# Optimization experiments

Hardware: AMD Instinct MI355X
Metric: run time of the kernel (lower is better)

## Reference

```python
import jax, jax.numpy as jnp
import numpy as np

EMB = 512
HEADS = 8

def setup_inputs() -> dict:
    key = jax.random.key(0)
    ks = jax.random.split(key, 6)
    x = jax.random.normal(ks[0], (8, 1024, EMB), dtype=jnp.float32)
    s = EMB ** -0.5
    Wq = jax.random.normal(ks[1], (EMB, EMB), dtype=jnp.float32) * s
    Wk = jax.random.normal(ks[2], (EMB, EMB), dtype=jnp.float32) * s
    Wv = jax.random.normal(ks[3], (EMB, EMB), dtype=jnp.float32) * s
    ln_gamma = jnp.ones((EMB,), dtype=jnp.float32)
    ln_beta = jnp.zeros((EMB,), dtype=jnp.float32)
    return {"x": x, "Wq": Wq, "Wk": Wk, "Wv": Wv, "ln_gamma": ln_gamma, "ln_beta": ln_beta}

def reference(x, Wq, Wk, Wv, ln_gamma, ln_beta):
    B, S, E = x.shape
    H = HEADS
    D = E // H
    scale = E ** -0.5  # note: source scales by emb_size**-0.5, not head_dim
    # projections (bias=False, torch Linear: x @ W.T)
    q = (x @ Wq.T).reshape(B, S, H, D).transpose(0, 2, 1, 3)  # [B,H,S,D]
    k = (x @ Wk.T).reshape(B, S, H, D).transpose(0, 2, 1, 3)
    v = (x @ Wv.T).reshape(B, S, H, D).transpose(0, 2, 1, 3)
    attn = jnp.einsum('bhqd,bhkd->bhqk', q, k) * scale
    attn = jax.nn.softmax(attn, axis=-1)
    out = jnp.einsum('bhqk,bhkd->bhqd', attn, v)
    out = out.transpose(0, 2, 1, 3).reshape(B, S, E)
    # LayerNorm (eps=1e-5, torch default)
    mu = jnp.mean(out, axis=-1, keepdims=True)
    var = jnp.var(out, axis=-1, keepdims=True)
    out = (out - mu) * jax.lax.rsqrt(var + 1e-5) * ln_gamma + ln_beta
    return out
```

## Files before the change

### kernel.cpp

```cpp
#include <hip/hip_runtime.h>
#include <hip/hip_bf16.h>

typedef __bf16 bf16_t;
typedef __bf16 bf16x4 __attribute__((ext_vector_type(4)));
typedef __bf16 bf16x8 __attribute__((ext_vector_type(8)));
typedef float  f32x4  __attribute__((ext_vector_type(4)));
typedef short  short4v __attribute__((ext_vector_type(4)));

#define GLL(gp, lp) __builtin_amdgcn_global_load_lds((const __attribute__((address_space(1))) void*)(gp), (__attribute__((address_space(3))) void*)(lp), 16, 0, 0)

__device__ __forceinline__ f32x4 mfma16x16x16_bf16(bf16x4 a, bf16x4 b, f32x4 c) {
#if __has_builtin(__builtin_amdgcn_mfma_f32_16x16x16_bf16)
    return __builtin_amdgcn_mfma_f32_16x16x16_bf16(a, b, c, 0, 0, 0);
#else
    return __builtin_amdgcn_mfma_f32_16x16x16bf16_1k(__builtin_bit_cast(short4v, a), __builtin_bit_cast(short4v, b), c, 0, 0, 0);
#endif
}

__device__ __forceinline__ float fexp2(float x) {
#if __has_builtin(__builtin_amdgcn_exp2f)
    return __builtin_amdgcn_exp2f(x);
#else
    return exp2f(x);
#endif
}

__global__ __launch_bounds__(256) void cvt_kernel(const float* __restrict__ x,
                                                  const float* __restrict__ wq,
                                                  const float* __restrict__ wk,
                                                  const float* __restrict__ wv,
                                                  bf16_t* __restrict__ xb,
                                                  bf16_t* __restrict__ wall) {
    const int TOT4 = 1245184;
    for (int i = blockIdx.x * blockDim.x + threadIdx.x; i < TOT4; i += gridDim.x * blockDim.x) {
        const float* src; bf16_t* dst; int off;
        if (i < 1048576) { src = x; dst = xb; off = i; }
        else {
            int j = i - 1048576;
            int wsel = j >> 16;
            off = j & 65535;
            src = (wsel == 0) ? wq : ((wsel == 1) ? wk : wv);
            dst = wall + ((size_t)wsel << 18);
        }
        float4 v = *(const float4*)(src + (size_t)off * 4);
        bf16x4 o = { (bf16_t)v.x, (bf16_t)v.y, (bf16_t)v.z, (bf16_t)v.w };
        *(bf16x4*)(dst + (size_t)off * 4) = o;
    }
}

__global__ __launch_bounds__(256) void proj_kernel(const bf16_t* __restrict__ xb,
                                                   const bf16_t* __restrict__ wall,
                                                   bf16_t* __restrict__ Qb,
                                                   bf16_t* __restrict__ Kb,
                                                   bf16_t* __restrict__ Vt) {
    __shared__ char psm[34816];

    const int tid = threadIdx.x;
    const int w = tid >> 6, lane = tid & 63;
    const int bx = blockIdx.x;
    const int nb = bx % 12, mb = bx / 12;
    const int n0 = nb * 128, m0 = mb * 128;
    const int wn = w & 1, wm = w >> 1;
    const int l15 = lane & 15, g = lane >> 4;

    const int srow = w * 32 + (lane >> 2);
    const int kcol = (((lane & 3) ^ ((lane >> 3) & 3)) << 3);
    const bf16_t* wsrc0 = wall + (size_t)(n0 + srow) * 512 + kcol;
    const bf16_t* xsrc0 = xb + (size_t)(m0 + srow) * 512 + kcol;

    f32x4 acc[4][4] = {};

    {
        bf16_t* lw = (bf16_t*)(psm) + w * 1024;
        bf16_t* lx = (bf16_t*)(psm + 8192) + w * 1024;
        GLL(wsrc0, lw);
        GLL(wsrc0 + 8192, lw + 512);
        GLL(xsrc0, lx);
        GLL(xsrc0 + 8192, lx + 512);
    }
    __syncthreads();

    const int s4 = (l15 >> 1) & 3;

    for (int kt = 0; kt < 16; ++kt) {
        const int buf = kt & 1;
        if (kt < 15) {
            const int ko = (kt + 1) * 32;
            bf16_t* lw = (bf16_t*)(psm + (buf ^ 1) * 16384) + w * 1024;
            bf16_t* lx = (bf16_t*)(psm + (buf ^ 1) * 16384 + 8192) + w * 1024;
            GLL(wsrc0 + ko, lw);
            GLL(wsrc0 + 8192 + ko, lw + 512);
            GLL(xsrc0 + ko, lx);
            GLL(xsrc0 + 8192 + ko, lx + 512);
        }
        const bf16_t* sW = (const bf16_t*)(psm + buf * 16384);
        const bf16_t* sX = (const bf16_t*)(psm + buf * 16384 + 8192);

        bf16x8 af[4], bfv[4];
#pragma unroll
        for (int ni = 0; ni < 4; ++ni)
            af[ni] = *(const bf16x8*)(sW + (wn * 64 + ni * 16 + l15) * 32 + ((g ^ s4) << 3));
#pragma unroll
        for (int mi = 0; mi < 4; ++mi)
            bfv[mi] = *(const bf16x8*)(sX + (wm * 64 + mi * 16 + l15) * 32 + ((g ^ s4) << 3));
#pragma unroll
        for (int ni = 0; ni < 4; ++ni)
#pragma unroll
            for (int mi = 0; mi < 4; ++mi)
                acc[ni][mi] = __builtin_amdgcn_mfma_f32_16x16x32_bf16(af[ni], bfv[mi], acc[ni][mi], 0, 0, 0);
        __syncthreads();
    }

    const int which = n0 >> 9;
    if (which < 2) {
        bf16_t* dst = (which == 0) ? Qb : Kb;
#pragma unroll
        for (int ni = 0; ni < 4; ++ni) {
#pragma unroll
            for (int mi = 0; mi < 4; ++mi) {
                int j = (n0 & 511) + wn * 64 + ni * 16 + g * 4;
                int h = j >> 6, dd = j & 63;
                int sb = m0 + wm * 64 + mi * 16 + l15;
                int b = sb >> 10, s = sb & 1023;
                bf16x4 o = { (bf16_t)acc[ni][mi][0], (bf16_t)acc[ni][mi][1],
                             (bf16_t)acc[ni][mi][2], (bf16_t)acc[ni][mi][3] };
                *(bf16x4*)(dst + ((size_t)((b * 8 + h) * 1024 + s)) * 64 + dd) = o;
            }
        }
    } else {
        bf16_t* ctile = (bf16_t*)psm;
#pragma unroll
        for (int ni = 0; ni < 4; ++ni)
#pragma unroll
            for (int mi = 0; mi < 4; ++mi)
#pragma unroll
                for (int r = 0; r < 4; ++r)
                    ctile[(wn * 64 + ni * 16 + g * 4 + r) * 136 + wm * 64 + mi * 16 + l15] =
                        (bf16_t)acc[ni][mi][r];
        __syncthreads();
        const int rr = tid >> 1, half = tid & 1;
        const int jv = (n0 & 511) + rr;
        const int hh = jv >> 6, dd = jv & 63;
        const int b = m0 >> 10, sb = (m0 & 1023) + half * 64;
        bf16_t* dst = Vt + ((size_t)((b * 8 + hh) * 64 + dd)) * 1024 + sb;
        const bf16_t* src = ctile + rr * 136 + half * 64;
#pragma unroll
        for (int u = 0; u < 8; ++u)
            *(bf16x8*)(dst + u * 8) = *(const bf16x8*)(src + u * 8);
    }
}

__global__ __launch_bounds__(512, 4) void attn_kernel(const bf16_t* __restrict__ Qb,
                                                      const bf16_t* __restrict__ Kb,
                                                      const bf16_t* __restrict__ Vt,
                                                      bf16_t* __restrict__ Ob) {
    __shared__ char smem[65536];
    const int tid = threadIdx.x;
    const int w = tid >> 6, lane = tid & 63;
    const int pipe = w >> 2, ws = w & 3;
    const int l15 = lane & 15, g = lane >> 4, l7 = lane & 7;

    const int bx = blockIdx.x;
    const int xcd = bx & 7, i = bx >> 3;
    const int head = xcd * 8 + (i & 7);
    const int qblk = i >> 3;
    const int q0 = qblk * 128 + ws * 32;

    const size_t hoff = (size_t)head << 16;
    const bf16_t* Qh = Qb + hoff;
    const char* Kh = (const char*)(Kb + hoff) + pipe * 65536;
    const char* Vh = (const char*)(Vt + hoff) + pipe * 1024;

    const float c2 = 0.06376390597f;

    bf16x8 qf[2][2];
#pragma unroll
    for (int qh = 0; qh < 2; ++qh) {
        const bf16_t* qp = Qh + (q0 + qh * 16 + l15) * 64 + g * 8;
        bf16x8 a = *(const bf16x8*)(qp);
        bf16x8 bq = *(const bf16x8*)(qp + 32);
#pragma unroll
        for (int j = 0; j < 8; ++j) {
            a[j] = (bf16_t)((float)a[j] * c2);
            bq[j] = (bf16_t)((float)bq[j] * c2);
        }
        qf[qh][0] = a; qf[qh][1] = bq;
    }

    const int srow = ws * 8 + (lane >> 3);
    const int sw16 = (l7 ^ ((lane >> 3) & 7)) << 4;
    const char* Ksrc = Kh + srow * 128 + sw16;
    const char* Vsrc = Vh + srow * 2048 + sw16;
    char* region = smem + pipe * 32768;
    char* dstK = region + ws * 1024;
    char* dstV = region + 8192 + ws * 1024;

    const int e0 = (l7 ^ g) << 4;
    const int f0 = (g << 3) ^ (l7 << 4);

    const f32x4 minit = { -4.0f, -4.0f, -4.0f, -4.0f };
    const int b = head >> 3, h = head & 7;

    f32x4 oacc[2][4] = {};
    float denom[2] = { 0.f, 0.f };

    GLL(Ksrc, dstK);
    GLL(Ksrc + 4096, dstK + 4096);
    GLL(Vsrc, dstV);
    GLL(Vsrc + 65536, dstV + 4096);
    __syncthreads();

    for (int c = 0; c < 8; ++c) {
        const int buf = c & 1;
        if (c < 7) {
            const int nbo = (buf ^ 1) * 16384;
            GLL(Ksrc + (c + 1) * 8192, dstK + nbo);
            GLL(Ksrc + (c + 1) * 8192 + 4096, dstK + nbo + 4096);
            GLL(Vsrc + (c + 1) * 128, dstV + nbo);
            GLL(Vsrc + (c + 1) * 128 + 65536, dstV + nbo + 4096);
        }
        const char* bK = region + buf * 16384;
        const char* bV = bK + 8192;

        bf16x4 pb[2][4];
#pragma unroll
        for (int sub = 0; sub < 4; ++sub) {
            const char* rowp = bK + (sub * 16 + l15) * 128;
            bf16x8 ka0 = *(const bf16x8*)(rowp + e0);
            bf16x8 ka1 = *(const bf16x8*)(rowp + (e0 ^ 64));
#pragma unroll
            for (int qh = 0; qh < 2; ++qh) {
                f32x4 st = __builtin_amdgcn_mfma_f32_16x16x32_bf16(ka0, qf[qh][0], minit, 0, 0, 0);
                st = __builtin_amdgcn_mfma_f32_16x16x32_bf16(ka1, qf[qh][1], st, 0, 0, 0);
                float p0 = fexp2(st[0]), p1 = fexp2(st[1]), p2 = fexp2(st[2]), p3 = fexp2(st[3]);
                denom[qh] += (p0 + p1) + (p2 + p3);
                bf16x4 pv = { (bf16_t)p0, (bf16_t)p1, (bf16_t)p2, (bf16_t)p3 };
                pb[qh][sub] = pv;
            }
        }

        __builtin_amdgcn_s_setprio(1);
#pragma unroll
        for (int dt = 0; dt < 4; ++dt) {
            const char* vrowp = bV + (dt * 16 + l15) * 128;
#pragma unroll
            for (int ks = 0; ks < 4; ++ks) {
                bf16x4 va = *(const bf16x4*)(vrowp + (f0 ^ (ks << 5)));
                oacc[0][dt] = mfma16x16x16_bf16(va, pb[0][ks], oacc[0][dt]);
                oacc[1][dt] = mfma16x16x16_bf16(va, pb[1][ks], oacc[1][dt]);
            }
        }
        __builtin_amdgcn_s_setprio(0);
        __syncthreads();
    }

    float dn[2];
#pragma unroll
    for (int qh = 0; qh < 2; ++qh) {
        float d0 = denom[qh];
        d0 += __shfl_xor(d0, 16);
        d0 += __shfl_xor(d0, 32);
        dn[qh] = d0;
    }

    if (pipe == 1) {
#pragma unroll
        for (int qh = 0; qh < 2; ++qh) {
#pragma unroll
            for (int dt = 0; dt < 4; ++dt)
                *(f32x4*)(smem + (((ws * 2 + qh) * 4) + dt) * 1024 + lane * 16) = oacc[qh][dt];
            *(float*)(smem + 32768 + (ws * 2 + qh) * 256 + lane * 4) = dn[qh];
        }
    }
    __syncthreads();
    if (pipe == 0) {
#pragma unroll
        for (int qh = 0; qh < 2; ++qh) {
            const float dp = *(const float*)(smem + 32768 + (ws * 2 + qh) * 256 + lane * 4);
            const float inv = 1.0f / (dn[qh] + dp);
            const int s = q0 + qh * 16 + l15;
            bf16_t* op = Ob + ((size_t)(b * 1024 + s)) * 512 + h * 64 + g * 4;
#pragma unroll
            for (int dt = 0; dt < 4; ++dt) {
                f32x4 o2 = *(const f32x4*)(smem + (((ws * 2 + qh) * 4) + dt) * 1024 + lane * 16);
                f32x4 t = oacc[qh][dt] + o2;
                bf16x4 o = { (bf16_t)(t[0] * inv), (bf16_t)(t[1] * inv),
                             (bf16_t)(t[2] * inv), (bf16_t)(t[3] * inv) };
                *(bf16x4*)(op + dt * 16) = o;
            }
        }
    }
}

__global__ __launch_bounds__(256) void ln_kernel(const bf16_t* __restrict__ O,
                                                 const float* __restrict__ gamma,
                                                 const float* __restrict__ beta,
                                                 float* __restrict__ out) {
    const int w = threadIdx.x >> 6, lane = threadIdx.x & 63;
    const int row = blockIdx.x * 4 + w;
    const bf16_t* rp = O + (size_t)row * 512 + lane * 8;
    bf16x8 v8 = *(const bf16x8*)rp;
    float v[8];
    float sum = 0.0f, sq = 0.0f;
#pragma unroll
    for (int i = 0; i < 8; ++i) { v[i] = (float)v8[i]; sum += v[i]; sq += v[i] * v[i]; }
#pragma unroll
    for (int msk = 1; msk < 64; msk <<= 1) {
        sum += __shfl_xor(sum, msk);
        sq  += __shfl_xor(sq, msk);
    }
    const float mean = sum * (1.0f / 512.0f);
    const float var = sq * (1.0f / 512.0f) - mean * mean;
    const float rs = rsqrtf(var + 1e-5f);
    float4 g0 = *(const float4*)(gamma + lane * 8);
    float4 g1 = *(const float4*)(gamma + lane * 8 + 4);
    float4 b0 = *(const float4*)(beta + lane * 8);
    float4 b1 = *(const float4*)(beta + lane * 8 + 4);
    float* op = out + (size_t)row * 512 + lane * 8;
    float4 o0, o1;
    o0.x = (v[0] - mean) * rs * g0.x + b0.x;
    o0.y = (v[1] - mean) * rs * g0.y + b0.y;
    o0.z = (v[2] - mean) * rs * g0.z + b0.z;
    o0.w = (v[3] - mean) * rs * g0.w + b0.w;
    o1.x = (v[4] - mean) * rs * g1.x + b1.x;
    o1.y = (v[5] - mean) * rs * g1.y + b1.y;
    o1.z = (v[6] - mean) * rs * g1.z + b1.z;
    o1.w = (v[7] - mean) * rs * g1.w + b1.w;
    *(float4*)op = o0;
    *(float4*)(op + 4) = o1;
}

extern "C" void kernel_launch(void* const* d_in, const int* in_sizes, int n_in,
                              void* d_out, int out_size, void* d_ws, size_t ws_size,
                              hipStream_t stream) {
    const float* x  = (const float*)d_in[0];
    const float* wq = (const float*)d_in[1];
    const float* wk = (const float*)d_in[2];
    const float* wv = (const float*)d_in[3];
    const float* gamma = (const float*)d_in[4];
    const float* beta  = (const float*)d_in[5];
    float* out = (float*)d_out;

    char* ws = (char*)d_ws;
    bf16_t* xb   = (bf16_t*)(ws);
    bf16_t* wall = (bf16_t*)(ws + 8388608);
    bf16_t* Qb   = (bf16_t*)(ws + 9961472);
    bf16_t* Kb   = (bf16_t*)(ws + 18350080);
    bf16_t* Vt   = (bf16_t*)(ws + 26738688);
    bf16_t* Ob   = (bf16_t*)(ws + 35127296);

    hipLaunchKernelGGL(cvt_kernel,  dim3(1024), dim3(256), 0, stream, x, wq, wk, wv, xb, wall);
    hipLaunchKernelGGL(proj_kernel, dim3(768),  dim3(256), 0, stream, xb, wall, Qb, Kb, Vt);
    hipLaunchKernelGGL(attn_kernel, dim3(512),  dim3(512), 0, stream, Qb, Kb, Vt, Ob);
    hipLaunchKernelGGL(ln_kernel,   dim3(2048), dim3(256), 0, stream, Ob, gamma, beta, out);
}
```

Measured before the change: 68.20 us.

## Drop split-KV dual-pipe attention in favor of single-pipe 256-thread blocks

Removes the intra-block split of the key range across two 4-wave pipes, so each block of 4 waves now walks all 16 KV chunks itself. This drops the shared-memory cross-pipe reduction of partial outputs and denominators, plus its extra barrier. LDS use per block is halved and the launch bound allows 5 blocks per CU. Each wave now has twice as many serial iterations, which lengthens the per-block critical path, and there are half as many waves in flight per CU for the same grid.

```diff
diff --git a/kernel.cpp b/kernel.cpp
--- a/kernel.cpp
+++ b/kernel.cpp
@@ -150,26 +150,24 @@
     }
 }
 
-__global__ __launch_bounds__(512, 4) void attn_kernel(const bf16_t* __restrict__ Qb,
+__global__ __launch_bounds__(256, 5) void attn_kernel(const bf16_t* __restrict__ Qb,
                                                       const bf16_t* __restrict__ Kb,
                                                       const bf16_t* __restrict__ Vt,
                                                       bf16_t* __restrict__ Ob) {
-    __shared__ char smem[65536];
+    __shared__ char smem[32768];
     const int tid = threadIdx.x;
     const int w = tid >> 6, lane = tid & 63;
-    const int pipe = w >> 2, ws = w & 3;
     const int l15 = lane & 15, g = lane >> 4, l7 = lane & 7;
 
     const int bx = blockIdx.x;
-    const int xcd = bx & 7, i = bx >> 3;
-    const int head = xcd * 8 + (i & 7);
-    const int qblk = i >> 3;
-    const int q0 = qblk * 128 + ws * 32;
+    const int head = (bx & 7) * 8 + ((bx >> 3) & 7);
+    const int qblk = bx >> 6;
+    const int q0 = qblk * 128 + w * 32;
 
     const size_t hoff = (size_t)head << 16;
     const bf16_t* Qh = Qb + hoff;
-    const char* Kh = (const char*)(Kb + hoff) + pipe * 65536;
-    const char* Vh = (const char*)(Vt + hoff) + pipe * 1024;
+    const char* Kh = (const char*)(Kb + hoff);
+    const char* Vh = (const char*)(Vt + hoff);
 
     const float c2 = 0.06376390597f;
 
@@ -187,13 +185,12 @@
         qf[qh][0] = a; qf[qh][1] = bq;
     }
 
-    const int srow = ws * 8 + (lane >> 3);
+    const int srow = w * 8 + (lane >> 3);
     const int sw16 = (l7 ^ ((lane >> 3) & 7)) << 4;
     const char* Ksrc = Kh + srow * 128 + sw16;
     const char* Vsrc = Vh + srow * 2048 + sw16;
-    char* region = smem + pipe * 32768;
-    char* dstK = region + ws * 1024;
-    char* dstV = region + 8192 + ws * 1024;
+    char* dstK = smem + w * 1024;
+    char* dstV = smem + 8192 + w * 1024;
 
     const int e0 = (l7 ^ g) << 4;
     const int f0 = (g << 3) ^ (l7 << 4);
@@ -210,16 +207,16 @@
     GLL(Vsrc + 65536, dstV + 4096);
     __syncthreads();
 
-    for (int c = 0; c < 8; ++c) {
+    for (int c = 0; c < 16; ++c) {
         const int buf = c & 1;
-        if (c < 7) {
+        if (c < 15) {
             const int nbo = (buf ^ 1) * 16384;
             GLL(Ksrc + (c + 1) * 8192, dstK + nbo);
             GLL(Ksrc + (c + 1) * 8192 + 4096, dstK + nbo + 4096);
             GLL(Vsrc + (c + 1) * 128, dstV + nbo);
             GLL(Vsrc + (c + 1) * 128 + 65536, dstV + nbo + 4096);
         }
-        const char* bK = region + buf * 16384;
+        const char* bK = smem + buf * 16384;
         const char* bV = bK + 8192;
 
         bf16x4 pb[2][4];
@@ -254,40 +251,19 @@
         __syncthreads();
     }
 
-    float dn[2];
 #pragma unroll
     for (int qh = 0; qh < 2; ++qh) {
         float d0 = denom[qh];
         d0 += __shfl_xor(d0, 16);
         d0 += __shfl_xor(d0, 32);
-        dn[qh] = d0;
-    }
-
-    if (pipe == 1) {
-#pragma unroll
-        for (int qh = 0; qh < 2; ++qh) {
-#pragma unroll
-            for (int dt = 0; dt < 4; ++dt)
-                *(f32x4*)(smem + (((ws * 2 + qh) * 4) + dt) * 1024 + lane * 16) = oacc[qh][dt];
-            *(float*)(smem + 32768 + (ws * 2 + qh) * 256 + lane * 4) = dn[qh];
-        }
-    }
-    __syncthreads();
-    if (pipe == 0) {
-#pragma unroll
-        for (int qh = 0; qh < 2; ++qh) {
-            const float dp = *(const float*)(smem + 32768 + (ws * 2 + qh) * 256 + lane * 4);
-            const float inv = 1.0f / (dn[qh] + dp);
-            const int s = q0 + qh * 16 + l15;
-            bf16_t* op = Ob + ((size_t)(b * 1024 + s)) * 512 + h * 64 + g * 4;
-#pragma unroll
-            for (int dt = 0; dt < 4; ++dt) {
-                f32x4 o2 = *(const f32x4*)(smem + (((ws * 2 + qh) * 4) + dt) * 1024 + lane * 16);
-                f32x4 t = oacc[qh][dt] + o2;
-                bf16x4 o = { (bf16_t)(t[0] * inv), (bf16_t)(t[1] * inv),
-                             (bf16_t)(t[2] * inv), (bf16_t)(t[3] * inv) };
-                *(bf16x4*)(op + dt * 16) = o;
-            }
+        const float inv = 1.0f / d0;
+        const int s = q0 + qh * 16 + l15;
+        bf16_t* op = Ob + ((size_t)(b * 1024 + s)) * 512 + h * 64 + g * 4;
+#pragma unroll
+        for (int dt = 0; dt < 4; ++dt) {
+            bf16x4 o = { (bf16_t)(oacc[qh][dt][0] * inv), (bf16_t)(oacc[qh][dt][1] * inv),
+                         (bf16_t)(oacc[qh][dt][2] * inv), (bf16_t)(oacc[qh][dt][3] * inv) };
+            *(bf16x4*)(op + dt * 16) = o;
         }
     }
 }
@@ -351,6 +327,6 @@
 
     hipLaunchKernelGGL(cvt_kernel,  dim3(1024), dim3(256), 0, stream, x, wq, wk, wv, xb, wall);
     hipLaunchKernelGGL(proj_kernel, dim3(768),  dim3(256), 0, stream, xb, wall, Qb, Kb, Vt);
-    hipLaunchKernelGGL(attn_kernel, dim3(512),  dim3(512), 0, stream, Qb, Kb, Vt, Ob);
+    hipLaunchKernelGGL(attn_kernel, dim3(512),  dim3(256), 0, stream, Qb, Kb, Vt, Ob);
     hipLaunchKernelGGL(ln_kernel,   dim3(2048), dim3(256), 0, stream, Ob, gamma, beta, out);
 }
```

Result: slower. 108.1 us (+58.4%).
